# Kernel tuning notes

Measured on AMD Instinct MI355X. Metric: run time of the kernel, lower is better.

Reference implementation:

```python
import jax, jax.numpy as jnp
import numpy as np

NUM_CONTEXT = 8  # context panels; +1 choice -> 9 panels, 72 ordered pairs (i != j)

_PAIRS = np.array([(i, j) for i in range(9) for j in range(9) if i != j], dtype=np.int32)
I_IDX = jnp.asarray(_PAIRS[:, 0])  # [72]
J_IDX = jnp.asarray(_PAIRS[:, 1])  # [72]


def setup_inputs() -> dict:
    key = jax.random.key(0)
    ks = jax.random.split(key, 10)
    B, C, F, H = 256, 8, 512, 256
    s_in = 1.0 / np.sqrt(2 * F)
    s_h = 1.0 / np.sqrt(H)
    return {
        "context_features": jax.random.normal(ks[0], (B, NUM_CONTEXT, F), jnp.float32),
        "choice_features": jax.random.normal(ks[1], (B, C, F), jnp.float32),
        "W1": jax.random.uniform(ks[2], (2 * F, H), jnp.float32, -s_in, s_in),
        "b1": jax.random.uniform(ks[3], (H,), jnp.float32, -s_in, s_in),
        "W2": jax.random.uniform(ks[4], (H, H), jnp.float32, -s_h, s_h),
        "b2": jax.random.uniform(ks[5], (H,), jnp.float32, -s_h, s_h),
        "W3": jax.random.uniform(ks[6], (H, H), jnp.float32, -s_h, s_h),
        "b3": jax.random.uniform(ks[7], (H,), jnp.float32, -s_h, s_h),
        "W4": jax.random.uniform(ks[8], (H, 1), jnp.float32, -s_h, s_h),
        "b4": jax.random.uniform(ks[9], (1,), jnp.float32, -s_h, s_h),
    }


def reference(context_features, choice_features, W1, b1, W2, b2, W3, b3, W4, b4):
    B, C, F = choice_features.shape[0], choice_features.shape[1], choice_features.shape[2]
    # panels[b, c, p, f]: 8 context panels + 1 choice panel per candidate choice
    ctx = jnp.broadcast_to(context_features[:, None, :, :], (B, C, NUM_CONTEXT, F))
    panels = jnp.concatenate([ctx, choice_features[:, :, None, :]], axis=2)  # [B,C,9,F]
    # all 72 ordered pairs (i != j), concatenated features -> [B,C,72,2F]
    pair = jnp.concatenate([panels[:, :, I_IDX, :], panels[:, :, J_IDX, :]], axis=-1)
    # g_theta MLP
    h = jax.nn.relu(pair @ W1 + b1)
    h = jax.nn.relu(h @ W2 + b2)        # [B,C,72,H]
    agg = h.mean(axis=2)                # [B,C,H]
    # f_phi MLP (dropout is identity in eval mode)
    g = jax.nn.relu(agg @ W3 + b3)
    score = g @ W4 + b4                 # [B,C,1]
    return score[..., 0]                # [B,C]
```

## Files before the change

kernel.cpp:

```cpp
#include <hip/hip_runtime.h>
#include <hip/hip_bf16.h>


typedef __bf16 bf16_t;
typedef bf16_t bf16x8 __attribute__((ext_vector_type(8)));
typedef bf16_t bf16x4 __attribute__((ext_vector_type(4)));
typedef float f32x4 __attribute__((ext_vector_type(4)));

#define MFMA16(a, b, c) __builtin_amdgcn_mfma_f32_16x16x32_bf16((a), (b), (c), 0, 0, 0)

__global__ __launch_bounds__(256) void prep_kernel(
    const float* __restrict__ W1, const float* __restrict__ W2,
    const float* __restrict__ W3, bf16_t* __restrict__ Wp,
    bf16_t* __restrict__ W2T, bf16_t* __restrict__ W3T) {
  __shared__ float Ts[64][65];
  const int b = blockIdx.x;
  const int t = threadIdx.x;
  const int r = t >> 6;
  const int c = t & 63;
  const float* srcP;
  bf16_t* dstP;
  int srcRow, srcCol, dr0, dc0, dstride;
  if (b < 64) {
    const int k0 = (b >> 3) * 64, j0 = (b & 7) * 64;
    srcP = W1; dstP = Wp; dstride = 512;
    srcRow = (j0 < 256) ? k0 : 512 + k0;
    srcCol = (j0 < 256) ? j0 : j0 - 256;
    dr0 = j0; dc0 = k0;
  } else if (b < 80) {
    const int s = b - 64;
    const int k0 = (s >> 2) * 64, n0 = (s & 3) * 64;
    srcP = W2; dstP = W2T; dstride = 256;
    srcRow = k0; srcCol = n0; dr0 = n0; dc0 = k0;
  } else {
    const int s = b - 80;
    const int k0 = (s >> 2) * 64, n0 = (s & 3) * 64;
    srcP = W3; dstP = W3T; dstride = 256;
    srcRow = k0; srcCol = n0; dr0 = n0; dc0 = k0;
  }
  for (int i = 0; i < 16; ++i) {
    const int a = i * 4 + r;
    Ts[a][c] = srcP[(size_t)(srcRow + a) * 256 + srcCol + c];
  }
  __syncthreads();
  for (int i = 0; i < 16; ++i) {
    const int j = i * 4 + r;
    dstP[(size_t)(dr0 + j) * dstride + dc0 + c] = (bf16_t)Ts[c][j];
  }
}

__global__ __launch_bounds__(512) void k2_kernel(
    const float* __restrict__ ctx, const float* __restrict__ cho,
    const bf16_t* __restrict__ Wp, const float* __restrict__ b1,
    const float* __restrict__ b2, const bf16_t* __restrict__ W2T,
    const bf16_t* __restrict__ W3T, const float* __restrict__ b3,
    const float* __restrict__ W4, const float* __restrict__ b4,
    float* __restrict__ out) {
  __shared__ char smem[118016];
  bf16_t (*UVs)[520] = (bf16_t(*)[520])smem;
  bf16_t (*Xs)[520]  = (bf16_t(*)[520])(smem + 16640);
  bf16_t (*h1)[264]  = (bf16_t(*)[264])(smem + 16640);
  float  (*S)[256]   = (float(*)[256])(smem + 16640);
  bf16_t (*Ag)[264]  = (bf16_t(*)[264])(smem + 16640 + 9216);
  float  (*red)[8]   = (float(*)[8])(smem + 16640 + 9216 + 8448);
  const int b = blockIdx.x;
  const int t = threadIdx.x;
  const int lane = t & 63;
  const int w = t >> 6;
  const int col = lane & 15;
  const int quad = lane >> 4;

  {
    const int row = t >> 5;
    const int c0 = (t & 31) * 16;
    const float* src = (row < 8) ? ctx + ((size_t)b * 8 + row) * 512
                                 : cho + ((size_t)b * 8 + (row - 8)) * 512;
    const f32x4 x0 = *(const f32x4*)(src + c0);
    const f32x4 x1 = *(const f32x4*)(src + c0 + 4);
    const f32x4 x2 = *(const f32x4*)(src + c0 + 8);
    const f32x4 x3 = *(const f32x4*)(src + c0 + 12);
    bf16x8 y0, y1;
    for (int e = 0; e < 4; ++e) { y0[e] = (bf16_t)x0[e]; y0[4 + e] = (bf16_t)x1[e]; }
    for (int e = 0; e < 4; ++e) { y1[e] = (bf16_t)x2[e]; y1[4 + e] = (bf16_t)x3[e]; }
    *(bf16x8*)(&Xs[row][c0]) = y0;
    *(bf16x8*)(&Xs[row][c0 + 8]) = y1;
  }
  __syncthreads();

  {
    f32x4 acc1[4] = {};
    for (int ks = 0; ks < 16; ++ks) {
      const int k = ks * 32 + quad * 8;
      const bf16x8 af = *(const bf16x8*)(&Xs[col][k]);
      for (int nt = 0; nt < 4; ++nt) {
        const int n = w * 64 + nt * 16 + col;
        const bf16x8 bfr = *(const bf16x8*)(Wp + (size_t)n * 512 + k);
        acc1[nt] = MFMA16(af, bfr, acc1[nt]);
      }
    }
    for (int nt = 0; nt < 4; ++nt) {
      const int n = w * 64 + nt * 16 + col;
      for (int reg = 0; reg < 4; ++reg)
        UVs[quad * 4 + reg][n] = (bf16_t)acc1[nt][reg];
    }
  }
  __syncthreads();

  if (t < 384) {
    const int sr = t >> 1;
    const int sc0 = (t & 1) * 128;
    const bf16_t* su = nullptr;
    const bf16_t* sv = nullptr;
    if (sr < 56) {
      const int i = sr / 7;
      const int jj = sr - i * 7;
      const int j = jj + (jj >= i ? 1 : 0);
      su = UVs[i];
      sv = UVs[j] + 256;
    } else if (sr >= 64) {
      const int ch = (sr - 64) >> 4;
      const int rr = (sr - 64) & 15;
      if (rr < 8) { su = UVs[8 + ch]; sv = UVs[rr] + 256; }
      else        { su = UVs[rr - 8]; sv = UVs[8 + ch] + 256; }
    }
    if (su) {
      for (int c = sc0; c < sc0 + 128; c += 8) {
        const bf16x8 u8 = *(const bf16x8*)(su + c);
        const bf16x8 v8 = *(const bf16x8*)(sv + c);
        const f32x4 bb0 = *(const f32x4*)(b1 + c);
        const f32x4 bb1 = *(const f32x4*)(b1 + c + 4);
        bf16x8 y;
        for (int e = 0; e < 4; ++e)
          y[e] = (bf16_t)fmaxf((float)u8[e] + (float)v8[e] + bb0[e], 0.0f);
        for (int e = 0; e < 4; ++e)
          y[4 + e] = (bf16_t)fmaxf((float)u8[4 + e] + (float)v8[4 + e] + bb1[e], 0.0f);
        *(bf16x8*)(&h1[sr][c]) = y;
      }
    } else {
      for (int c = sc0; c < sc0 + 128; c += 8)
        *(bf16x8*)(&h1[sr][c]) = (bf16x8)0.0f;
    }
  }
  __syncthreads();

  const int mtb = (w & 1) * 6;
  const int q = w >> 1;
  f32x4 acc[6][4] = {};
  for (int ks = 0; ks < 8; ++ks) {
    const int k = ks * 32 + quad * 8;
    bf16x8 af[6], bfr[4];
    for (int mt = 0; mt < 6; ++mt)
      af[mt] = *(const bf16x8*)(&h1[(mtb + mt) * 16 + col][k]);
    for (int nt = 0; nt < 4; ++nt) {
      const int n = q * 64 + nt * 16 + col;
      bfr[nt] = *(const bf16x8*)(W2T + (size_t)n * 256 + k);
    }
    for (int mt = 0; mt < 6; ++mt)
      for (int nt = 0; nt < 4; ++nt)
        acc[mt][nt] = MFMA16(af[mt], bfr[nt], acc[mt][nt]);
  }
  __syncthreads();

  for (int nt = 0; nt < 4; ++nt) {
    const int n = q * 64 + nt * 16 + col;
    const float b2c = b2[n];
    float sctx = 0.0f;
    for (int mt = 0; mt < 6; ++mt) {
      const int gm = mtb + mt;
      float s = 0.0f;
      for (int reg = 0; reg < 4; ++reg) {
        const int row = gm * 16 + quad * 4 + reg;
        if (row < 56 || row >= 64) s += fmaxf(acc[mt][nt][reg] + b2c, 0.0f);
      }
      s += __shfl_xor(s, 16);
      s += __shfl_xor(s, 32);
      if (gm < 4) {
        sctx += s;
      } else if (lane < 16) {
        S[1 + (gm - 4)][n] = s;
      }
    }
    if (mtb == 0 && lane < 16) S[0][n] = sctx;
  }
  __syncthreads();
  {
    const int ch = t >> 6;
    const int n0 = (t & 63) * 4;
    bf16x4 y;
    for (int e = 0; e < 4; ++e)
      y[e] = (bf16_t)((S[0][n0 + e] + S[1 + ch][n0 + e]) * (1.0f / 72.0f));
    *(bf16x4*)(&Ag[ch][n0]) = y;
    *(bf16x4*)(&Ag[8 + ch][n0]) = (bf16x4)0.0f;
  }
  __syncthreads();
  f32x4 acc2[2] = {};
  for (int ks = 0; ks < 8; ++ks) {
    const int k = ks * 32 + quad * 8;
    const bf16x8 af = *(const bf16x8*)(&Ag[col][k]);
    for (int nt = 0; nt < 2; ++nt) {
      const int n = w * 32 + nt * 16 + col;
      const bf16x8 bfr = *(const bf16x8*)(W3T + (size_t)n * 256 + k);
      acc2[nt] = MFMA16(af, bfr, acc2[nt]);
    }
  }
  for (int reg = 0; reg < 4; ++reg) {
    float pr = 0.0f;
    for (int nt = 0; nt < 2; ++nt) {
      const int n = w * 32 + nt * 16 + col;
      pr += fmaxf(acc2[nt][reg] + b3[n], 0.0f) * W4[n];
    }
    pr += __shfl_xor(pr, 1);
    pr += __shfl_xor(pr, 2);
    pr += __shfl_xor(pr, 4);
    pr += __shfl_xor(pr, 8);
    if (col == 0 && quad < 2) red[w][quad * 4 + reg] = pr;
  }
  __syncthreads();
  if (t < 8) {
    float sc = b4[0];
    for (int ww = 0; ww < 8; ++ww) sc += red[ww][t];
    out[b * 8 + t] = sc;
  }
}

extern "C" void kernel_launch(void* const* d_in, const int* in_sizes, int n_in,
                              void* d_out, int out_size, void* d_ws, size_t ws_size,
                              hipStream_t stream) {
  (void)in_sizes; (void)n_in; (void)out_size; (void)ws_size;
  const float* ctx = (const float*)d_in[0];
  const float* cho = (const float*)d_in[1];
  const float* W1  = (const float*)d_in[2];
  const float* b1  = (const float*)d_in[3];
  const float* W2  = (const float*)d_in[4];
  const float* b2  = (const float*)d_in[5];
  const float* W3  = (const float*)d_in[6];
  const float* b3  = (const float*)d_in[7];
  const float* W4  = (const float*)d_in[8];
  const float* b4  = (const float*)d_in[9];
  char* ws = (char*)d_ws;
  bf16_t* Wp   = (bf16_t*)(ws + 0);
  bf16_t* W2T  = (bf16_t*)(ws + 524288);
  bf16_t* W3T  = (bf16_t*)(ws + 655360);
  float*  out  = (float*)d_out;

  prep_kernel<<<dim3(96), dim3(256), 0, stream>>>(W1, W2, W3, Wp, W2T, W3T);
  k2_kernel<<<dim3(256), dim3(512), 0, stream>>>(ctx, cho, Wp, b1, b2, W2T, W3T,
                                                 b3, W4, b4, out);
}
```

Before: 110.9 us.

## Fuse weight prep and main kernel via cooperative launch with grid sync

Merges the weight transpose/convert kernel into the main kernel. The first 96 blocks do the bf16 weight transposes, then all 256 blocks meet at a grid-wide barrier before the MLP work. The per-block input loads are issued before the barrier so their latency overlaps the prep phase. This removes a kernel launch and the gap between kernels, at the cost of a cooperative launch and a grid sync. It also requires all 256 blocks, each using about 118 KB of LDS, to be resident at once.

```diff
diff --git a/kernel.cpp b/kernel.cpp
--- a/kernel.cpp
+++ b/kernel.cpp
@@ -1,5 +1,8 @@
 #include <hip/hip_runtime.h>
 #include <hip/hip_bf16.h>
+#include <hip/hip_cooperative_groups.h>
+
+namespace cg = cooperative_groups;
 
 
 typedef __bf16 bf16_t;
@@ -9,55 +12,17 @@
 
 #define MFMA16(a, b, c) __builtin_amdgcn_mfma_f32_16x16x32_bf16((a), (b), (c), 0, 0, 0)
 
-__global__ __launch_bounds__(256) void prep_kernel(
+__global__ __launch_bounds__(512) void fused_kernel(
+    const float* __restrict__ ctx, const float* __restrict__ cho,
     const float* __restrict__ W1, const float* __restrict__ W2,
     const float* __restrict__ W3, bf16_t* __restrict__ Wp,
-    bf16_t* __restrict__ W2T, bf16_t* __restrict__ W3T) {
-  __shared__ float Ts[64][65];
-  const int b = blockIdx.x;
-  const int t = threadIdx.x;
-  const int r = t >> 6;
-  const int c = t & 63;
-  const float* srcP;
-  bf16_t* dstP;
-  int srcRow, srcCol, dr0, dc0, dstride;
-  if (b < 64) {
-    const int k0 = (b >> 3) * 64, j0 = (b & 7) * 64;
-    srcP = W1; dstP = Wp; dstride = 512;
-    srcRow = (j0 < 256) ? k0 : 512 + k0;
-    srcCol = (j0 < 256) ? j0 : j0 - 256;
-    dr0 = j0; dc0 = k0;
-  } else if (b < 80) {
-    const int s = b - 64;
-    const int k0 = (s >> 2) * 64, n0 = (s & 3) * 64;
-    srcP = W2; dstP = W2T; dstride = 256;
-    srcRow = k0; srcCol = n0; dr0 = n0; dc0 = k0;
-  } else {
-    const int s = b - 80;
-    const int k0 = (s >> 2) * 64, n0 = (s & 3) * 64;
-    srcP = W3; dstP = W3T; dstride = 256;
-    srcRow = k0; srcCol = n0; dr0 = n0; dc0 = k0;
-  }
-  for (int i = 0; i < 16; ++i) {
-    const int a = i * 4 + r;
-    Ts[a][c] = srcP[(size_t)(srcRow + a) * 256 + srcCol + c];
-  }
-  __syncthreads();
-  for (int i = 0; i < 16; ++i) {
-    const int j = i * 4 + r;
-    dstP[(size_t)(dr0 + j) * dstride + dc0 + c] = (bf16_t)Ts[c][j];
-  }
-}
-
-__global__ __launch_bounds__(512) void k2_kernel(
-    const float* __restrict__ ctx, const float* __restrict__ cho,
-    const bf16_t* __restrict__ Wp, const float* __restrict__ b1,
-    const float* __restrict__ b2, const bf16_t* __restrict__ W2T,
-    const bf16_t* __restrict__ W3T, const float* __restrict__ b3,
-    const float* __restrict__ W4, const float* __restrict__ b4,
-    float* __restrict__ out) {
+    bf16_t* __restrict__ W2T, bf16_t* __restrict__ W3T,
+    const float* __restrict__ b1, const float* __restrict__ b2,
+    const float* __restrict__ b3, const float* __restrict__ W4,
+    const float* __restrict__ b4, float* __restrict__ out) {
   __shared__ char smem[118016];
   bf16_t (*UVs)[520] = (bf16_t(*)[520])smem;
+  float  (*Ts)[65]   = (float(*)[65])smem;
   bf16_t (*Xs)[520]  = (bf16_t(*)[520])(smem + 16640);
   bf16_t (*h1)[264]  = (bf16_t(*)[264])(smem + 16640);
   float  (*S)[256]   = (float(*)[256])(smem + 16640);
@@ -70,20 +35,57 @@
   const int col = lane & 15;
   const int quad = lane >> 4;
 
+  const int xrow = t >> 5;
+  const int xc0 = (t & 31) * 16;
+  const float* xsrc = (xrow < 8) ? ctx + ((size_t)b * 8 + xrow) * 512
+                                 : cho + ((size_t)b * 8 + (xrow - 8)) * 512;
+  const f32x4 x0 = *(const f32x4*)(xsrc + xc0);
+  const f32x4 x1 = *(const f32x4*)(xsrc + xc0 + 4);
+  const f32x4 x2 = *(const f32x4*)(xsrc + xc0 + 8);
+  const f32x4 x3 = *(const f32x4*)(xsrc + xc0 + 12);
+
+  if (b < 96) {
+    const int r = t >> 6;
+    const int c = t & 63;
+    const float* srcP;
+    bf16_t* dstP;
+    int srcRow, srcCol, dr0, dc0, dstride;
+    if (b < 64) {
+      const int k0 = (b >> 3) * 64, j0 = (b & 7) * 64;
+      srcP = W1; dstP = Wp; dstride = 512;
+      srcRow = (j0 < 256) ? k0 : 512 + k0;
+      srcCol = (j0 < 256) ? j0 : j0 - 256;
+      dr0 = j0; dc0 = k0;
+    } else if (b < 80) {
+      const int s = b - 64;
+      const int k0 = (s >> 2) * 64, n0 = (s & 3) * 64;
+      srcP = W2; dstP = W2T; dstride = 256;
+      srcRow = k0; srcCol = n0; dr0 = n0; dc0 = k0;
+    } else {
+      const int s = b - 80;
+      const int k0 = (s >> 2) * 64, n0 = (s & 3) * 64;
+      srcP = W3; dstP = W3T; dstride = 256;
+      srcRow = k0; srcCol = n0; dr0 = n0; dc0 = k0;
+    }
+    for (int i = 0; i < 8; ++i) {
+      const int a = i * 8 + r;
+      Ts[a][c] = srcP[(size_t)(srcRow + a) * 256 + srcCol + c];
+    }
+    __syncthreads();
+    for (int i = 0; i < 8; ++i) {
+      const int j = i * 8 + r;
+      dstP[(size_t)(dr0 + j) * dstride + dc0 + c] = (bf16_t)Ts[c][j];
+    }
+    __threadfence();
+  }
+  cg::this_grid().sync();
+
   {
-    const int row = t >> 5;
-    const int c0 = (t & 31) * 16;
-    const float* src = (row < 8) ? ctx + ((size_t)b * 8 + row) * 512
-                                 : cho + ((size_t)b * 8 + (row - 8)) * 512;
-    const f32x4 x0 = *(const f32x4*)(src + c0);
-    const f32x4 x1 = *(const f32x4*)(src + c0 + 4);
-    const f32x4 x2 = *(const f32x4*)(src + c0 + 8);
-    const f32x4 x3 = *(const f32x4*)(src + c0 + 12);
     bf16x8 y0, y1;
     for (int e = 0; e < 4; ++e) { y0[e] = (bf16_t)x0[e]; y0[4 + e] = (bf16_t)x1[e]; }
     for (int e = 0; e < 4; ++e) { y1[e] = (bf16_t)x2[e]; y1[4 + e] = (bf16_t)x3[e]; }
-    *(bf16x8*)(&Xs[row][c0]) = y0;
-    *(bf16x8*)(&Xs[row][c0 + 8]) = y1;
+    *(bf16x8*)(&Xs[xrow][xc0]) = y0;
+    *(bf16x8*)(&Xs[xrow][xc0 + 8]) = y1;
   }
   __syncthreads();
 
@@ -243,7 +245,8 @@
   bf16_t* W3T  = (bf16_t*)(ws + 655360);
   float*  out  = (float*)d_out;
 
-  prep_kernel<<<dim3(96), dim3(256), 0, stream>>>(W1, W2, W3, Wp, W2T, W3T);
-  k2_kernel<<<dim3(256), dim3(512), 0, stream>>>(ctx, cho, Wp, b1, b2, W2T, W3T,
-                                                 b3, W4, b4, out);
+  void* args[] = {&ctx, &cho, &W1, &W2, &W3, &Wp, &W2T, &W3T,
+                  &b1, &b2, &b3, &W4, &b4, &out};
+  hipLaunchCooperativeKernel((const void*)fused_kernel, dim3(256), dim3(512),
+                             args, 0, stream);
 }
```

New measurement: 172.1 us. 1.55x slower.
